# Kernel optimization log

Hardware: AMD Instinct MI355X
Metric: run time of the kernel (lower is better)

## Reference

```python
import jax, jax.numpy as jnp
import numpy as np

B, T, D = 16, 2048, 1024
N_E, D_E = 8, 64


def setup_inputs() -> dict:
    key = jax.random.key(0)
    ks = jax.random.split(key, 8)
    h_seq = jax.random.normal(ks[0], (B, T, D), dtype=jnp.float32)
    entity_keys = jax.random.normal(ks[1], (N_E, D), dtype=jnp.float32) * 0.02
    # input_proj: Linear(D -> D_E)
    Wi = jax.random.normal(ks[2], (D_E, D), dtype=jnp.float32) * (1.0 / np.sqrt(D))
    bi = jnp.zeros((D_E,), dtype=jnp.float32)
    # GRUCell(D_E, D_E): weight_ih (3*D_E, D_E), weight_hh (3*D_E, D_E)
    s = 1.0 / np.sqrt(D_E)
    W_ih = jax.random.uniform(ks[3], (3 * D_E, D_E), minval=-s, maxval=s, dtype=jnp.float32)
    W_hh = jax.random.uniform(ks[4], (3 * D_E, D_E), minval=-s, maxval=s, dtype=jnp.float32)
    b_ih = jax.random.uniform(ks[5], (3 * D_E,), minval=-s, maxval=s, dtype=jnp.float32)
    b_hh = jax.random.uniform(ks[6], (3 * D_E,), minval=-s, maxval=s, dtype=jnp.float32)
    e0 = jnp.zeros((N_E, D_E), dtype=jnp.float32)
    return {"h_seq": h_seq, "entity_keys": entity_keys, "Wi": Wi, "bi": bi,
            "W_ih": W_ih, "W_hh": W_hh, "b_ih": b_ih, "b_hh": b_hh, "e0": e0}


def _entity_scan(h_seq, entity_keys, Wi, bi, W_ih, W_hh, b_ih, b_hh, e0):
    Bq, Tq, Dq = h_seq.shape
    d_e = e0.shape[-1]
    h_proj = jnp.einsum('btd,ed->bte', h_seq, Wi) + bi          # (B,T,D_E)
    logits = jnp.einsum('btd,ed->bte', h_seq, entity_keys) / jnp.sqrt(jnp.float32(Dq))
    route_w = jax.nn.softmax(logits, axis=-1)                    # (B,T,N_E)

    def step(state, xs):
        w_t, hp_t = xs                                           # (B,N_E), (B,D_E)
        inp = w_t[:, :, None] * hp_t[:, None, :]                 # (B,N_E,D_E)
        gx = jnp.einsum('bnd,gd->bng', inp, W_ih) + b_ih         # (B,N_E,3*D_E)
        gh = jnp.einsum('bnd,gd->bng', state, W_hh) + b_hh
        r = jax.nn.sigmoid(gx[..., :d_e] + gh[..., :d_e])
        z = jax.nn.sigmoid(gx[..., d_e:2 * d_e] + gh[..., d_e:2 * d_e])
        n = jnp.tanh(gx[..., 2 * d_e:] + r * gh[..., 2 * d_e:])
        new = (1.0 - z) * n + z * state
        return new, new

    init = jnp.broadcast_to(e0[None], (Bq,) + e0.shape)
    xs = (jnp.swapaxes(route_w, 0, 1), jnp.swapaxes(h_proj, 0, 1))  # time-major
    _, stack = jax.lax.scan(step, init, xs)                      # (T,B,N_E,D_E)
    entity_stack = jnp.swapaxes(stack, 0, 1)                     # (B,T,N_E,D_E)
    entity_seq = entity_stack.reshape(Bq, Tq, -1)                # concat read mode
    return entity_seq, entity_stack


def reference(h_seq, entity_keys, Wi, bi, W_ih, W_hh, b_ih, b_hh, e0):
    return _entity_scan(h_seq, entity_keys, Wi, bi, W_ih, W_hh, b_ih, b_hh, e0)
```

## Files before the change

kernel.cpp:

```cpp
#include <hip/hip_runtime.h>
#include <hip/hip_bf16.h>


constexpr int B_  = 16;
constexpr int T_  = 2048;
constexpr int D_  = 1024;
constexpr int NE  = 8;
constexpr int DE  = 64;
constexpr int G3  = 192;
constexpr int ROWS = B_ * T_;
constexpr int OUT1OFF = ROWS * NE * DE;

typedef __attribute__((ext_vector_type(2))) float f32x2;
typedef __attribute__((ext_vector_type(4))) float f32x4;

__device__ __forceinline__ void pkacc(f32x2& acc, f32x2 w, f32x2 s) {
    asm("v_pk_fma_f32 %0, %1, %2, %0" : "+v"(acc) : "v"(w), "v"(s));
}

__global__ __launch_bounds__(256) void wt_kernel(
    const float* __restrict__ Wi, float* __restrict__ WT4)
{
    const int o  = blockIdx.x;
    const int dq = threadIdx.x;
    const float4 v = *(const float4*)&Wi[o * D_ + dq * 4];
    *(float4*)&WT4[(dq * 64 + o) * 4] = v;
}

constexpr int RPB = 32;
constexpr int CH  = 128;

__global__ __launch_bounds__(256) void proj_kernel(
    const float* __restrict__ h,   const float* __restrict__ ek,
    const float* __restrict__ WT4, const float* __restrict__ bi,
    const float* __restrict__ Wih,
    float* __restrict__ Pout, float* __restrict__ wout)
{
    __shared__ float hch[RPB][CH];
    __shared__ float hp[RPB][DE];
    __shared__ float lg[RPB][NE];

    const int tid = threadIdx.x;
    const int brow = blockIdx.x * RPB;
    const int w = tid >> 6;
    const int o = tid & 63;
    const int n  = o & 7;
    const int sl = o >> 3;

    float acc[8], accl[8];
#pragma unroll
    for (int r = 0; r < 8; ++r) { acc[r] = 0.f; accl[r] = 0.f; }

    for (int kc = 0; kc < D_; kc += CH) {
        __syncthreads();
#pragma unroll
        for (int i = 0; i < 4; ++i) {
            int idx = tid + i * 256;
            int lr = idx >> 5;
            int c4 = (idx & 31) * 4;
            *(float4*)&hch[lr][c4] =
                *(const float4*)&h[(size_t)(brow + lr) * D_ + kc + c4];
        }
        __syncthreads();

        for (int d4 = 0; d4 < CH / 4; ++d4) {
            const float4 wt = *(const float4*)&WT4[((kc >> 2) + d4) * 256 + (o << 2)];
#pragma unroll
            for (int r = 0; r < 8; ++r) {
                const float4 h4 = *(const float4*)&hch[w * 8 + r][d4 * 4];
                acc[r] = fmaf(wt.x, h4.x,
                         fmaf(wt.y, h4.y,
                         fmaf(wt.z, h4.z,
                         fmaf(wt.w, h4.w, acc[r]))));
            }
        }
#pragma unroll
        for (int i4 = 0; i4 < 4; ++i4) {
            const int dl = sl * 16 + i4 * 4;
            const float4 e4 = *(const float4*)&ek[n * D_ + kc + dl];
#pragma unroll
            for (int r = 0; r < 8; ++r) {
                const float4 h4 = *(const float4*)&hch[w * 8 + r][dl];
                accl[r] = fmaf(e4.x, h4.x,
                          fmaf(e4.y, h4.y,
                          fmaf(e4.z, h4.z,
                          fmaf(e4.w, h4.w, accl[r]))));
            }
        }
    }

    const float biv = bi[o];
#pragma unroll
    for (int r = 0; r < 8; ++r) hp[w * 8 + r][o] = acc[r] + biv;

#pragma unroll
    for (int r = 0; r < 8; ++r) {
        accl[r] += __shfl_xor(accl[r], 8);
        accl[r] += __shfl_xor(accl[r], 16);
        accl[r] += __shfl_xor(accl[r], 32);
    }
    if (sl == 0) {
#pragma unroll
        for (int r = 0; r < 8; ++r) lg[w * 8 + r][n] = accl[r] * 0.03125f;
    }
    __syncthreads();

    if (tid < RPB) {
        const int lr = tid;
        float v[NE];
        float m = -1e30f;
#pragma unroll
        for (int e = 0; e < NE; ++e) { v[e] = lg[lr][e]; m = fmaxf(m, v[e]); }
        float s = 0.f;
#pragma unroll
        for (int e = 0; e < NE; ++e) { v[e] = __expf(v[e] - m); s += v[e]; }
        const float inv = 1.f / s;
#pragma unroll
        for (int e = 0; e < NE; ++e)
            wout[(size_t)(brow + lr) * NE + e] = v[e] * inv;
    }

    if (tid < G3) {
        const int k = tid;
        for (int lr0 = 0; lr0 < RPB; lr0 += 8) {
            float pacc[8];
#pragma unroll
            for (int r = 0; r < 8; ++r) pacc[r] = 0.f;
            for (int d4 = 0; d4 < DE / 4; ++d4) {
                const float4 wv = *(const float4*)&Wih[k * DE + d4 * 4];
#pragma unroll
                for (int r = 0; r < 8; ++r) {
                    const float4 h4 = *(const float4*)&hp[lr0 + r][d4 * 4];
                    pacc[r] = fmaf(wv.x, h4.x,
                              fmaf(wv.y, h4.y,
                              fmaf(wv.z, h4.z,
                              fmaf(wv.w, h4.w, pacc[r]))));
                }
            }
#pragma unroll
            for (int r = 0; r < 8; ++r)
                Pout[(size_t)(brow + lr0 + r) * G3 + k] = pacc[r];
        }
    }
}

#define DW(pre, base, q) \
    const f32x4 pre##q = *(const f32x4*)&Whh[(size_t)(base + j) * 64 + 4 * q];
#define DW16(pre, base) \
    DW(pre, base, 0)  DW(pre, base, 1)  DW(pre, base, 2)  DW(pre, base, 3)  \
    DW(pre, base, 4)  DW(pre, base, 5)  DW(pre, base, 6)  DW(pre, base, 7)  \
    DW(pre, base, 8)  DW(pre, base, 9)  DW(pre, base, 10) DW(pre, base, 11) \
    DW(pre, base, 12) DW(pre, base, 13) DW(pre, base, 14) DW(pre, base, 15)

#define MACQ(q) { \
    const f32x4 s4 = *(const f32x4*)&s_l[4 * (q)]; \
    const f32x2 lo = s4.lo, hi = s4.hi; \
    pkacc(aR, wr##q.lo, lo); pkacc(aR, wr##q.hi, hi); \
    pkacc(aZ, wz##q.lo, lo); pkacc(aZ, wz##q.hi, hi); \
    pkacc(aN, wn##q.lo, lo); pkacc(aN, wn##q.hi, hi); }
#define MAC16() \
    MACQ(0)  MACQ(1)  MACQ(2)  MACQ(3)  MACQ(4)  MACQ(5)  MACQ(6)  MACQ(7) \
    MACQ(8)  MACQ(9)  MACQ(10) MACQ(11) MACQ(12) MACQ(13) MACQ(14) MACQ(15)

__global__ __launch_bounds__(64, 1) void scan_kernel(
    const float* __restrict__ P,   const float* __restrict__ route,
    const float* __restrict__ Whh, const float* __restrict__ bih,
    const float* __restrict__ bhh, const float* __restrict__ e0,
    float* __restrict__ out)
{
    __shared__ __align__(16) float s_l[DE];

    const int g   = blockIdx.x;
    const int xcd = g & 7;
    const int ii  = g >> 3;
    const int b   = xcd + 8 * (ii & 1);
    const int n   = ii >> 1;
    const int j   = threadIdx.x;

    DW16(wr, 0)
    DW16(wz, 64)
    DW16(wn, 128)

    const float Br   = bih[j] + bhh[j];
    const float Bz   = bih[64 + j] + bhh[64 + j];
    const float bin_ = bih[128 + j];
    const float bhn_ = bhh[128 + j];

    const size_t row0 = (size_t)b * T_;
    float s_reg = e0[n * DE + j];
    s_l[j] = s_reg;

    const float* Pb = P + row0 * G3;
    const float* wb = route + row0 * NE + n;
    float* op = out + row0 * (size_t)(NE * DE) + n * DE + j;

    float pr0 = Pb[j],            pr1 = Pb[G3 + j];
    float pz0 = Pb[64 + j],       pz1 = Pb[G3 + 64 + j];
    float pn0 = Pb[128 + j],      pn1 = Pb[G3 + 128 + j];
    float wv0 = wb[0],            wv1 = wb[NE];

    for (int t0 = 0; t0 < T_; t0 += 2) {
        const int tb = (t0 + 2 < T_) ? (t0 + 2) : t0;
        const float qr0 = Pb[(size_t)(tb) * G3 + j];
        const float qz0 = Pb[(size_t)(tb) * G3 + 64 + j];
        const float qn0 = Pb[(size_t)(tb) * G3 + 128 + j];
        const float qw0 = wb[tb * NE];
        const float qr1 = Pb[(size_t)(tb + 1) * G3 + j];
        const float qz1 = Pb[(size_t)(tb + 1) * G3 + 64 + j];
        const float qn1 = Pb[(size_t)(tb + 1) * G3 + 128 + j];
        const float qw1 = wb[(tb + 1) * NE];

#pragma unroll
        for (int i = 0; i < 2; ++i) {
            const float pri = i ? pr1 : pr0;
            const float pzi = i ? pz1 : pz0;
            const float pni = i ? pn1 : pn0;
            const float wvi = i ? wv1 : wv0;

            f32x2 aR = {0.f, 0.f}, aZ = {0.f, 0.f}, aN = {0.f, 0.f};
            MAC16()

            const float argR = (aR.x + aR.y) + fmaf(wvi, pri, Br);
            const float argZ = (aZ.x + aZ.y) + fmaf(wvi, pzi, Bz);
            const float rr = __builtin_amdgcn_rcpf(1.f + __expf(-argR));
            const float zz = __builtin_amdgcn_rcpf(1.f + __expf(-argZ));
            const float u  = fmaf(wvi, pni, bin_);
            const float v  = (aN.x + aN.y) + bhn_;
            const float x  = fmaf(rr, v, u);
            const float nn = fmaf(2.f, __builtin_amdgcn_rcpf(1.f + __expf(-2.f * x)), -1.f);
            const float snew = fmaf(zz, s_reg - nn, nn);
            s_reg = snew;
            s_l[j] = snew;
            op[(size_t)(t0 + i) * (NE * DE)] = snew;
        }

        pr0 = qr0; pz0 = qz0; pn0 = qn0; wv0 = qw0;
        pr1 = qr1; pz1 = qz1; pn1 = qn1; wv1 = qw1;
    }
}

__global__ __launch_bounds__(256) void copy_kernel(
    const float4* __restrict__ src, float4* __restrict__ dst, int n4)
{
    int i = blockIdx.x * 256 + threadIdx.x;
    const int stride = gridDim.x * 256;
    for (; i < n4; i += stride) dst[i] = src[i];
}

extern "C" void kernel_launch(void* const* d_in, const int* in_sizes, int n_in,
                              void* d_out, int out_size, void* d_ws, size_t ws_size,
                              hipStream_t stream) {
    const float* h_seq = (const float*)d_in[0];
    const float* ek    = (const float*)d_in[1];
    const float* Wi    = (const float*)d_in[2];
    const float* bi    = (const float*)d_in[3];
    const float* Wih   = (const float*)d_in[4];
    const float* Whh   = (const float*)d_in[5];
    const float* bih   = (const float*)d_in[6];
    const float* bhh   = (const float*)d_in[7];
    const float* e0    = (const float*)d_in[8];
    float* out = (float*)d_out;

    const size_t need = (size_t)ROWS * (G3 + NE) * sizeof(float)
                      + (size_t)DE * D_ * sizeof(float);
    float* wbuf;
    if (ws_size >= need) {
        wbuf = (float*)d_ws;
    } else {
        wbuf = out + OUT1OFF;
    }
    float* Pbuf = wbuf + (size_t)ROWS * NE;
    float* WT4  = Pbuf + (size_t)ROWS * G3;

    wt_kernel<<<DE, 256, 0, stream>>>(Wi, WT4);
    proj_kernel<<<ROWS / RPB, 256, 0, stream>>>(h_seq, ek, WT4, bi, Wih, Pbuf, wbuf);
    scan_kernel<<<B_ * NE, 64, 0, stream>>>(Pbuf, wbuf, Whh, bih, bhh, e0, out);
    copy_kernel<<<2048, 256, 0, stream>>>((const float4*)out, (float4*)(out + OUT1OFF),
                                          OUT1OFF / 4);
}
```

Baseline: 1.121 ms.

## Split GRU gates across three wavefronts and write both outputs directly from scan

The scan kernel now runs 192 threads per block, one wavefront per gate (r, z, n). Each wavefront computes a single 64-wide mat-vec with its gate weights held in registers, and the gates are exchanged through double-buffered shared memory with one barrier per timestep. This cuts the serial per-step work per lane to a third, at the cost of a block-wide barrier on every step. When the workspace is large enough, the second wavefront also writes the duplicate output, so the separate copy kernel is skipped.

```diff
diff --git a/kernel.cpp b/kernel.cpp
--- a/kernel.cpp
+++ b/kernel.cpp
@@ -144,98 +144,92 @@
     }
 }
 
-#define DW(pre, base, q) \
-    const f32x4 pre##q = *(const f32x4*)&Whh[(size_t)(base + j) * 64 + 4 * q];
-#define DW16(pre, base) \
-    DW(pre, base, 0)  DW(pre, base, 1)  DW(pre, base, 2)  DW(pre, base, 3)  \
-    DW(pre, base, 4)  DW(pre, base, 5)  DW(pre, base, 6)  DW(pre, base, 7)  \
-    DW(pre, base, 8)  DW(pre, base, 9)  DW(pre, base, 10) DW(pre, base, 11) \
-    DW(pre, base, 12) DW(pre, base, 13) DW(pre, base, 14) DW(pre, base, 15)
+#define DW(q) const f32x4 w##q = *(const f32x4*)&Whh[(size_t)base * 64 + 4 * (q)];
+#define DW16() \
+    DW(0)  DW(1)  DW(2)  DW(3)  DW(4)  DW(5)  DW(6)  DW(7) \
+    DW(8)  DW(9)  DW(10) DW(11) DW(12) DW(13) DW(14) DW(15)
 
 #define MACQ(q) { \
-    const f32x4 s4 = *(const f32x4*)&s_l[4 * (q)]; \
-    const f32x2 lo = s4.lo, hi = s4.hi; \
-    pkacc(aR, wr##q.lo, lo); pkacc(aR, wr##q.hi, hi); \
-    pkacc(aZ, wz##q.lo, lo); pkacc(aZ, wz##q.hi, hi); \
-    pkacc(aN, wn##q.lo, lo); pkacc(aN, wn##q.hi, hi); }
+    const f32x4 s4 = *(const f32x4*)&s_own[wid][4 * (q)]; \
+    pkacc(acc, w##q.lo, s4.lo); pkacc(acc, w##q.hi, s4.hi); }
 #define MAC16() \
     MACQ(0)  MACQ(1)  MACQ(2)  MACQ(3)  MACQ(4)  MACQ(5)  MACQ(6)  MACQ(7) \
     MACQ(8)  MACQ(9)  MACQ(10) MACQ(11) MACQ(12) MACQ(13) MACQ(14) MACQ(15)
 
-__global__ __launch_bounds__(64, 1) void scan_kernel(
+__global__ __launch_bounds__(192, 1) void scan_kernel(
     const float* __restrict__ P,   const float* __restrict__ route,
     const float* __restrict__ Whh, const float* __restrict__ bih,
     const float* __restrict__ bhh, const float* __restrict__ e0,
-    float* __restrict__ out)
-{
-    __shared__ __align__(16) float s_l[DE];
+    float* __restrict__ out, int write1)
+{
+    __shared__ __align__(16) float s_own[3][DE];
+    __shared__ float ex[2][4][DE];
 
     const int g   = blockIdx.x;
     const int xcd = g & 7;
     const int ii  = g >> 3;
     const int b   = xcd + 8 * (ii & 1);
     const int n   = ii >> 1;
-    const int j   = threadIdx.x;
-
-    DW16(wr, 0)
-    DW16(wz, 64)
-    DW16(wn, 128)
-
-    const float Br   = bih[j] + bhh[j];
-    const float Bz   = bih[64 + j] + bhh[64 + j];
-    const float bin_ = bih[128 + j];
-    const float bhn_ = bhh[128 + j];
+    const int tid = threadIdx.x;
+    const int wid = tid >> 6;
+    const int j   = tid & 63;
+    const int base = wid * DE + j;
+
+    DW16()
+
+    const float Bc   = bih[base] + bhh[base];
+    const float bin_ = bih[base];
+    const float bhn_ = bhh[base];
 
     const size_t row0 = (size_t)b * T_;
     float s_reg = e0[n * DE + j];
-    s_l[j] = s_reg;
-
-    const float* Pb = P + row0 * G3;
-    const float* wb = route + row0 * NE + n;
+    s_own[wid][j] = s_reg;
+
+    const float* Pb = P + row0 * G3 + base;
+    const float* rb = route + row0 * NE + n;
     float* op = out + row0 * (size_t)(NE * DE) + n * DE + j;
 
-    float pr0 = Pb[j],            pr1 = Pb[G3 + j];
-    float pz0 = Pb[64 + j],       pz1 = Pb[G3 + 64 + j];
-    float pn0 = Pb[128 + j],      pn1 = Pb[G3 + 128 + j];
-    float wv0 = wb[0],            wv1 = wb[NE];
-
-    for (int t0 = 0; t0 < T_; t0 += 2) {
-        const int tb = (t0 + 2 < T_) ? (t0 + 2) : t0;
-        const float qr0 = Pb[(size_t)(tb) * G3 + j];
-        const float qz0 = Pb[(size_t)(tb) * G3 + 64 + j];
-        const float qn0 = Pb[(size_t)(tb) * G3 + 128 + j];
-        const float qw0 = wb[tb * NE];
-        const float qr1 = Pb[(size_t)(tb + 1) * G3 + j];
-        const float qz1 = Pb[(size_t)(tb + 1) * G3 + 64 + j];
-        const float qn1 = Pb[(size_t)(tb + 1) * G3 + 128 + j];
-        const float qw1 = wb[(tb + 1) * NE];
-
-#pragma unroll
-        for (int i = 0; i < 2; ++i) {
-            const float pri = i ? pr1 : pr0;
-            const float pzi = i ? pz1 : pz0;
-            const float pni = i ? pn1 : pn0;
-            const float wvi = i ? wv1 : wv0;
-
-            f32x2 aR = {0.f, 0.f}, aZ = {0.f, 0.f}, aN = {0.f, 0.f};
-            MAC16()
-
-            const float argR = (aR.x + aR.y) + fmaf(wvi, pri, Br);
-            const float argZ = (aZ.x + aZ.y) + fmaf(wvi, pzi, Bz);
-            const float rr = __builtin_amdgcn_rcpf(1.f + __expf(-argR));
-            const float zz = __builtin_amdgcn_rcpf(1.f + __expf(-argZ));
-            const float u  = fmaf(wvi, pni, bin_);
-            const float v  = (aN.x + aN.y) + bhn_;
-            const float x  = fmaf(rr, v, u);
-            const float nn = fmaf(2.f, __builtin_amdgcn_rcpf(1.f + __expf(-2.f * x)), -1.f);
-            const float snew = fmaf(zz, s_reg - nn, nn);
-            s_reg = snew;
-            s_l[j] = snew;
-            op[(size_t)(t0 + i) * (NE * DE)] = snew;
-        }
-
-        pr0 = qr0; pz0 = qz0; pn0 = qn0; wv0 = qw0;
-        pr1 = qr1; pz1 = qz1; pn1 = qn1; wv1 = qw1;
+    float p0 = Pb[0], p1 = Pb[G3];
+    float wv0 = rb[0], wv1 = rb[NE];
+
+    int buf = 0;
+
+    for (int t = 0; t < T_; ++t) {
+        const int tn = (t + 2 < T_) ? (t + 2) : t;
+        const float pnx  = Pb[(size_t)tn * G3];
+        const float wnx  = rb[(size_t)tn * NE];
+
+        f32x2 acc = {0.f, 0.f};
+        MAC16()
+        const float gh = acc.x + acc.y;
+        const float gx = fmaf(wv0, p0, (wid == 2) ? bin_ : Bc);
+
+        if (wid == 2) {
+            ex[buf][2][j] = gx;
+            ex[buf][3][j] = gh + bhn_;
+        } else {
+            const float sg = __builtin_amdgcn_rcpf(1.f + __expf(-(gx + gh)));
+            ex[buf][wid][j] = sg;
+        }
+
+        asm volatile("s_waitcnt lgkmcnt(0)" ::: "memory");
+        __builtin_amdgcn_s_barrier();
+
+        const float rr = ex[buf][0][j];
+        const float zz = ex[buf][1][j];
+        const float u  = ex[buf][2][j];
+        const float v  = ex[buf][3][j];
+        const float x  = fmaf(rr, v, u);
+        const float nn = fmaf(2.f, __builtin_amdgcn_rcpf(1.f + __expf(-2.f * x)), -1.f);
+        const float snew = fmaf(zz, s_reg - nn, nn);
+        s_reg = snew;
+        s_own[wid][j] = snew;
+
+        if (wid == 0) op[(size_t)t * (NE * DE)] = snew;
+        else if (write1 && wid == 1) op[OUT1OFF + (size_t)t * (NE * DE)] = snew;
+
+        p0 = p1; p1 = pnx; wv0 = wv1; wv1 = wnx;
+        buf ^= 1;
     }
 }
 
@@ -264,17 +258,23 @@
     const size_t need = (size_t)ROWS * (G3 + NE) * sizeof(float)
                       + (size_t)DE * D_ * sizeof(float);
     float* wbuf;
+    int write1;
     if (ws_size >= need) {
         wbuf = (float*)d_ws;
+        write1 = 1;
     } else {
         wbuf = out + OUT1OFF;
+        write1 = 0;
     }
     float* Pbuf = wbuf + (size_t)ROWS * NE;
     float* WT4  = Pbuf + (size_t)ROWS * G3;
 
     wt_kernel<<<DE, 256, 0, stream>>>(Wi, WT4);
     proj_kernel<<<ROWS / RPB, 256, 0, stream>>>(h_seq, ek, WT4, bi, Wih, Pbuf, wbuf);
-    scan_kernel<<<B_ * NE, 64, 0, stream>>>(Pbuf, wbuf, Whh, bih, bhh, e0, out);
-    copy_kernel<<<2048, 256, 0, stream>>>((const float4*)out, (float4*)(out + OUT1OFF),
-                                          OUT1OFF / 4);
-}
+    scan_kernel<<<B_ * NE, 192, 0, stream>>>(Pbuf, wbuf, Whh, bih, bhh, e0, out, write1);
+
+    if (!write1) {
+        copy_kernel<<<2048, 256, 0, stream>>>((const float4*)out,
+                                              (float4*)(out + OUT1OFF), OUT1OFF / 4);
+    }
+}
```

New measurement: 1.386 ms. 1.24x slower.

## Write both scan outputs directly and split FMA accumulator chains

Applied to the files above, without the earlier changes.

The scan kernel now writes each new state to both output tensors when the workspace is large enough, so the separate copy kernel launch and its full read and write pass over the output are skipped. The packed-FMA accumulators are split into two independent chains per gate to shorten the serial dependency in the recurrent matvec. Empty asm constraints pin the W_hh weights in registers, and launch bounds move to a waves-per-EU attribute. In exchange the serial scan issues twice as many global stores, which may slow its critical path.

```diff
diff --git a/kernel.cpp b/kernel.cpp
--- a/kernel.cpp
+++ b/kernel.cpp
@@ -145,28 +145,36 @@
 }
 
 #define DW(pre, base, q) \
-    const f32x4 pre##q = *(const f32x4*)&Whh[(size_t)(base + j) * 64 + 4 * q];
+    f32x4 pre##q = *(const f32x4*)&Whh[(size_t)(base + j) * 64 + 4 * (q)];
 #define DW16(pre, base) \
     DW(pre, base, 0)  DW(pre, base, 1)  DW(pre, base, 2)  DW(pre, base, 3)  \
     DW(pre, base, 4)  DW(pre, base, 5)  DW(pre, base, 6)  DW(pre, base, 7)  \
     DW(pre, base, 8)  DW(pre, base, 9)  DW(pre, base, 10) DW(pre, base, 11) \
     DW(pre, base, 12) DW(pre, base, 13) DW(pre, base, 14) DW(pre, base, 15)
 
+#define KA(pre, q) asm volatile("" : "+v"(pre##q));
+#define KA16(pre) \
+    KA(pre, 0)  KA(pre, 1)  KA(pre, 2)  KA(pre, 3)  KA(pre, 4)  KA(pre, 5) \
+    KA(pre, 6)  KA(pre, 7)  KA(pre, 8)  KA(pre, 9)  KA(pre, 10) KA(pre, 11) \
+    KA(pre, 12) KA(pre, 13) KA(pre, 14) KA(pre, 15)
+
 #define MACQ(q) { \
     const f32x4 s4 = *(const f32x4*)&s_l[4 * (q)]; \
     const f32x2 lo = s4.lo, hi = s4.hi; \
-    pkacc(aR, wr##q.lo, lo); pkacc(aR, wr##q.hi, hi); \
-    pkacc(aZ, wz##q.lo, lo); pkacc(aZ, wz##q.hi, hi); \
-    pkacc(aN, wn##q.lo, lo); pkacc(aN, wn##q.hi, hi); }
+    pkacc(aRa, wr##q.lo, lo); pkacc(aRb, wr##q.hi, hi); \
+    pkacc(aZa, wz##q.lo, lo); pkacc(aZb, wz##q.hi, hi); \
+    pkacc(aNa, wn##q.lo, lo); pkacc(aNb, wn##q.hi, hi); }
 #define MAC16() \
     MACQ(0)  MACQ(1)  MACQ(2)  MACQ(3)  MACQ(4)  MACQ(5)  MACQ(6)  MACQ(7) \
     MACQ(8)  MACQ(9)  MACQ(10) MACQ(11) MACQ(12) MACQ(13) MACQ(14) MACQ(15)
 
-__global__ __launch_bounds__(64, 1) void scan_kernel(
+__global__ __launch_bounds__(64)
+__attribute__((amdgpu_waves_per_eu(1, 1)))
+void scan_kernel(
     const float* __restrict__ P,   const float* __restrict__ route,
     const float* __restrict__ Whh, const float* __restrict__ bih,
     const float* __restrict__ bhh, const float* __restrict__ e0,
-    float* __restrict__ out)
+    float* __restrict__ out, int write1)
 {
     __shared__ __align__(16) float s_l[DE];
 
@@ -180,6 +188,7 @@
     DW16(wr, 0)
     DW16(wz, 64)
     DW16(wn, 128)
+    KA16(wr) KA16(wz) KA16(wn)
 
     const float Br   = bih[j] + bhh[j];
     const float Bz   = bih[64 + j] + bhh[64 + j];
@@ -194,10 +203,10 @@
     const float* wb = route + row0 * NE + n;
     float* op = out + row0 * (size_t)(NE * DE) + n * DE + j;
 
-    float pr0 = Pb[j],            pr1 = Pb[G3 + j];
-    float pz0 = Pb[64 + j],       pz1 = Pb[G3 + 64 + j];
-    float pn0 = Pb[128 + j],      pn1 = Pb[G3 + 128 + j];
-    float wv0 = wb[0],            wv1 = wb[NE];
+    float pr0 = Pb[j],       pr1 = Pb[G3 + j];
+    float pz0 = Pb[64 + j],  pz1 = Pb[G3 + 64 + j];
+    float pn0 = Pb[128 + j], pn1 = Pb[G3 + 128 + j];
+    float wv0 = wb[0],       wv1 = wb[NE];
 
     for (int t0 = 0; t0 < T_; t0 += 2) {
         const int tb = (t0 + 2 < T_) ? (t0 + 2) : t0;
@@ -217,9 +226,12 @@
             const float pni = i ? pn1 : pn0;
             const float wvi = i ? wv1 : wv0;
 
-            f32x2 aR = {0.f, 0.f}, aZ = {0.f, 0.f}, aN = {0.f, 0.f};
+            f32x2 aRa = {0.f, 0.f}, aRb = {0.f, 0.f};
+            f32x2 aZa = {0.f, 0.f}, aZb = {0.f, 0.f};
+            f32x2 aNa = {0.f, 0.f}, aNb = {0.f, 0.f};
             MAC16()
 
+            const f32x2 aR = aRa + aRb, aZ = aZa + aZb, aN = aNa + aNb;
             const float argR = (aR.x + aR.y) + fmaf(wvi, pri, Br);
             const float argZ = (aZ.x + aZ.y) + fmaf(wvi, pzi, Bz);
             const float rr = __builtin_amdgcn_rcpf(1.f + __expf(-argR));
@@ -232,6 +244,7 @@
             s_reg = snew;
             s_l[j] = snew;
             op[(size_t)(t0 + i) * (NE * DE)] = snew;
+            if (write1) op[OUT1OFF + (size_t)(t0 + i) * (NE * DE)] = snew;
         }
 
         pr0 = qr0; pz0 = qz0; pn0 = qn0; wv0 = qw0;
@@ -264,17 +277,23 @@
     const size_t need = (size_t)ROWS * (G3 + NE) * sizeof(float)
                       + (size_t)DE * D_ * sizeof(float);
     float* wbuf;
+    int write1;
     if (ws_size >= need) {
         wbuf = (float*)d_ws;
+        write1 = 1;
     } else {
         wbuf = out + OUT1OFF;
+        write1 = 0;
     }
     float* Pbuf = wbuf + (size_t)ROWS * NE;
     float* WT4  = Pbuf + (size_t)ROWS * G3;
 
     wt_kernel<<<DE, 256, 0, stream>>>(Wi, WT4);
     proj_kernel<<<ROWS / RPB, 256, 0, stream>>>(h_seq, ek, WT4, bi, Wih, Pbuf, wbuf);
-    scan_kernel<<<B_ * NE, 64, 0, stream>>>(Pbuf, wbuf, Whh, bih, bhh, e0, out);
-    copy_kernel<<<2048, 256, 0, stream>>>((const float4*)out, (float4*)(out + OUT1OFF),
-                                          OUT1OFF / 4);
-}
+    scan_kernel<<<B_ * NE, 64, 0, stream>>>(Pbuf, wbuf, Whh, bih, bhh, e0, out, write1);
+
+    if (!write1) {
+        copy_kernel<<<2048, 256, 0, stream>>>((const float4*)out,
+                                              (float4*)(out + OUT1OFF), OUT1OFF / 4);
+    }
+}
```

After: 1.447 ms. 1.29x slower.

## Restructure projection kernel to hold h rows in registers and drop weight transpose

Applied to the files above, without the earlier changes.

The projection kernel now assigns each thread one row with a quarter of the D dimension, keeping 64 floats of h in registers while looping over the 72 output columns (Wi plus entity keys), which are read as wave-uniform broadcasts. Partial sums across the four waves are combined with shared-memory atomics, and the W_ih projection runs per row from registers. The separate Wi transpose kernel and its workspace are removed. The intent is to drop the LDS staging and one launch, at the cost of high register pressure from the large register arrays and atomic contention in LDS.

```diff
diff --git a/kernel.cpp b/kernel.cpp
--- a/kernel.cpp
+++ b/kernel.cpp
@@ -18,134 +18,104 @@
     asm("v_pk_fma_f32 %0, %1, %2, %0" : "+v"(acc) : "v"(w), "v"(s));
 }
 
-__global__ __launch_bounds__(256) void wt_kernel(
-    const float* __restrict__ Wi, float* __restrict__ WT4)
-{
-    const int o  = blockIdx.x;
-    const int dq = threadIdx.x;
-    const float4 v = *(const float4*)&Wi[o * D_ + dq * 4];
-    *(float4*)&WT4[(dq * 64 + o) * 4] = v;
-}
-
-constexpr int RPB = 32;
-constexpr int CH  = 128;
+constexpr int PRJ_ROWS = 64;
 
 __global__ __launch_bounds__(256) void proj_kernel(
     const float* __restrict__ h,   const float* __restrict__ ek,
-    const float* __restrict__ WT4, const float* __restrict__ bi,
+    const float* __restrict__ Wi,  const float* __restrict__ bi,
     const float* __restrict__ Wih,
     float* __restrict__ Pout, float* __restrict__ wout)
 {
-    __shared__ float hch[RPB][CH];
-    __shared__ float hp[RPB][DE];
-    __shared__ float lg[RPB][NE];
-
-    const int tid = threadIdx.x;
-    const int brow = blockIdx.x * RPB;
-    const int w = tid >> 6;
-    const int o = tid & 63;
-    const int n  = o & 7;
-    const int sl = o >> 3;
-
-    float acc[8], accl[8];
-#pragma unroll
-    for (int r = 0; r < 8; ++r) { acc[r] = 0.f; accl[r] = 0.f; }
-
-    for (int kc = 0; kc < D_; kc += CH) {
-        __syncthreads();
-#pragma unroll
-        for (int i = 0; i < 4; ++i) {
-            int idx = tid + i * 256;
-            int lr = idx >> 5;
-            int c4 = (idx & 31) * 4;
-            *(float4*)&hch[lr][c4] =
-                *(const float4*)&h[(size_t)(brow + lr) * D_ + kc + c4];
-        }
-        __syncthreads();
-
-        for (int d4 = 0; d4 < CH / 4; ++d4) {
-            const float4 wt = *(const float4*)&WT4[((kc >> 2) + d4) * 256 + (o << 2)];
-#pragma unroll
-            for (int r = 0; r < 8; ++r) {
-                const float4 h4 = *(const float4*)&hch[w * 8 + r][d4 * 4];
-                acc[r] = fmaf(wt.x, h4.x,
-                         fmaf(wt.y, h4.y,
-                         fmaf(wt.z, h4.z,
-                         fmaf(wt.w, h4.w, acc[r]))));
+    __shared__ float hp_l[72][PRJ_ROWS];
+
+    const int tid  = threadIdx.x;
+    const int w    = tid >> 6;
+    const int r    = tid & 63;
+    const int brow = blockIdx.x * PRJ_ROWS;
+
+    for (int i = tid; i < 72 * PRJ_ROWS; i += 256) ((float*)hp_l)[i] = 0.f;
+    __syncthreads();
+
+    const float* hrow = h + (size_t)(brow + r) * D_ + w * 256;
+
+    for (int kc = 0; kc < 4; ++kc) {
+        float4 hs[16];
+#pragma unroll
+        for (int i = 0; i < 16; ++i)
+            hs[i] = *(const float4*)&hrow[kc * 64 + i * 4];
+
+        for (int o = 0; o < 72; ++o) {
+            const float* wrow = (o < 64)
+                ? (Wi  + (size_t)o * D_        + w * 256 + kc * 64)
+                : (ek  + (size_t)(o - 64) * D_ + w * 256 + kc * 64);
+            float a0 = 0.f, a1 = 0.f, a2 = 0.f, a3 = 0.f;
+#pragma unroll
+            for (int i = 0; i < 16; i += 4) {
+                const float4 w0 = *(const float4*)&wrow[(i + 0) * 4];
+                const float4 w1 = *(const float4*)&wrow[(i + 1) * 4];
+                const float4 w2 = *(const float4*)&wrow[(i + 2) * 4];
+                const float4 w3 = *(const float4*)&wrow[(i + 3) * 4];
+                a0 = fmaf(w0.x, hs[i+0].x, fmaf(w0.y, hs[i+0].y,
+                     fmaf(w0.z, hs[i+0].z, fmaf(w0.w, hs[i+0].w, a0))));
+                a1 = fmaf(w1.x, hs[i+1].x, fmaf(w1.y, hs[i+1].y,
+                     fmaf(w1.z, hs[i+1].z, fmaf(w1.w, hs[i+1].w, a1))));
+                a2 = fmaf(w2.x, hs[i+2].x, fmaf(w2.y, hs[i+2].y,
+                     fmaf(w2.z, hs[i+2].z, fmaf(w2.w, hs[i+2].w, a2))));
+                a3 = fmaf(w3.x, hs[i+3].x, fmaf(w3.y, hs[i+3].y,
+                     fmaf(w3.z, hs[i+3].z, fmaf(w3.w, hs[i+3].w, a3))));
             }
-        }
-#pragma unroll
-        for (int i4 = 0; i4 < 4; ++i4) {
-            const int dl = sl * 16 + i4 * 4;
-            const float4 e4 = *(const float4*)&ek[n * D_ + kc + dl];
-#pragma unroll
-            for (int r = 0; r < 8; ++r) {
-                const float4 h4 = *(const float4*)&hch[w * 8 + r][dl];
-                accl[r] = fmaf(e4.x, h4.x,
-                          fmaf(e4.y, h4.y,
-                          fmaf(e4.z, h4.z,
-                          fmaf(e4.w, h4.w, accl[r]))));
-            }
-        }
-    }
-
-    const float biv = bi[o];
-#pragma unroll
-    for (int r = 0; r < 8; ++r) hp[w * 8 + r][o] = acc[r] + biv;
-
-#pragma unroll
-    for (int r = 0; r < 8; ++r) {
-        accl[r] += __shfl_xor(accl[r], 8);
-        accl[r] += __shfl_xor(accl[r], 16);
-        accl[r] += __shfl_xor(accl[r], 32);
-    }
-    if (sl == 0) {
-#pragma unroll
-        for (int r = 0; r < 8; ++r) lg[w * 8 + r][n] = accl[r] * 0.03125f;
+            atomicAdd(&hp_l[o][r], (a0 + a1) + (a2 + a3));
+        }
     }
     __syncthreads();
 
-    if (tid < RPB) {
-        const int lr = tid;
+    if (tid < PRJ_ROWS) {
         float v[NE];
         float m = -1e30f;
 #pragma unroll
-        for (int e = 0; e < NE; ++e) { v[e] = lg[lr][e]; m = fmaxf(m, v[e]); }
+        for (int e = 0; e < NE; ++e) {
+            v[e] = hp_l[64 + e][tid] * 0.03125f;
+            m = fmaxf(m, v[e]);
+        }
         float s = 0.f;
 #pragma unroll
         for (int e = 0; e < NE; ++e) { v[e] = __expf(v[e] - m); s += v[e]; }
         const float inv = 1.f / s;
 #pragma unroll
         for (int e = 0; e < NE; ++e)
-            wout[(size_t)(brow + lr) * NE + e] = v[e] * inv;
-    }
-
-    if (tid < G3) {
-        const int k = tid;
-        for (int lr0 = 0; lr0 < RPB; lr0 += 8) {
-            float pacc[8];
-#pragma unroll
-            for (int r = 0; r < 8; ++r) pacc[r] = 0.f;
-            for (int d4 = 0; d4 < DE / 4; ++d4) {
-                const float4 wv = *(const float4*)&Wih[k * DE + d4 * 4];
-#pragma unroll
-                for (int r = 0; r < 8; ++r) {
-                    const float4 h4 = *(const float4*)&hp[lr0 + r][d4 * 4];
-                    pacc[r] = fmaf(wv.x, h4.x,
-                              fmaf(wv.y, h4.y,
-                              fmaf(wv.z, h4.z,
-                              fmaf(wv.w, h4.w, pacc[r]))));
-                }
-            }
-#pragma unroll
-            for (int r = 0; r < 8; ++r)
-                Pout[(size_t)(brow + lr0 + r) * G3 + k] = pacc[r];
-        }
+            wout[(size_t)(brow + tid) * NE + e] = v[e] * inv;
+    }
+
+    float hpr[DE];
+#pragma unroll
+    for (int k = 0; k < DE; ++k)
+        hpr[k] = hp_l[k][r] + bi[k];
+
+    float* prow = Pout + (size_t)(brow + r) * G3;
+    for (int o2 = 48 * w; o2 < 48 * w + 48; ++o2) {
+        const float* wr2 = Wih + (size_t)o2 * DE;
+        float a0 = 0.f, a1 = 0.f, a2 = 0.f, a3 = 0.f;
+#pragma unroll
+        for (int i = 0; i < 16; i += 4) {
+            const float4 w0 = *(const float4*)&wr2[(i + 0) * 4];
+            const float4 w1 = *(const float4*)&wr2[(i + 1) * 4];
+            const float4 w2 = *(const float4*)&wr2[(i + 2) * 4];
+            const float4 w3 = *(const float4*)&wr2[(i + 3) * 4];
+            a0 = fmaf(w0.x, hpr[(i+0)*4+0], fmaf(w0.y, hpr[(i+0)*4+1],
+                 fmaf(w0.z, hpr[(i+0)*4+2], fmaf(w0.w, hpr[(i+0)*4+3], a0))));
+            a1 = fmaf(w1.x, hpr[(i+1)*4+0], fmaf(w1.y, hpr[(i+1)*4+1],
+                 fmaf(w1.z, hpr[(i+1)*4+2], fmaf(w1.w, hpr[(i+1)*4+3], a1))));
+            a2 = fmaf(w2.x, hpr[(i+2)*4+0], fmaf(w2.y, hpr[(i+2)*4+1],
+                 fmaf(w2.z, hpr[(i+2)*4+2], fmaf(w2.w, hpr[(i+2)*4+3], a2))));
+            a3 = fmaf(w3.x, hpr[(i+3)*4+0], fmaf(w3.y, hpr[(i+3)*4+1],
+                 fmaf(w3.z, hpr[(i+3)*4+2], fmaf(w3.w, hpr[(i+3)*4+3], a3))));
+        }
+        prow[o2] = (a0 + a1) + (a2 + a3);
     }
 }
 
 #define DW(pre, base, q) \
-    const f32x4 pre##q = *(const f32x4*)&Whh[(size_t)(base + j) * 64 + 4 * q];
+    const f32x4 pre##q = *(const f32x4*)&Whh[(size_t)(base + j) * 64 + 4 * (q)];
 #define DW16(pre, base) \
     DW(pre, base, 0)  DW(pre, base, 1)  DW(pre, base, 2)  DW(pre, base, 3)  \
     DW(pre, base, 4)  DW(pre, base, 5)  DW(pre, base, 6)  DW(pre, base, 7)  \
@@ -261,8 +231,7 @@
     const float* e0    = (const float*)d_in[8];
     float* out = (float*)d_out;
 
-    const size_t need = (size_t)ROWS * (G3 + NE) * sizeof(float)
-                      + (size_t)DE * D_ * sizeof(float);
+    const size_t need = (size_t)ROWS * (G3 + NE) * sizeof(float);
     float* wbuf;
     if (ws_size >= need) {
         wbuf = (float*)d_ws;
@@ -270,10 +239,8 @@
         wbuf = out + OUT1OFF;
     }
     float* Pbuf = wbuf + (size_t)ROWS * NE;
-    float* WT4  = Pbuf + (size_t)ROWS * G3;
-
-    wt_kernel<<<DE, 256, 0, stream>>>(Wi, WT4);
-    proj_kernel<<<ROWS / RPB, 256, 0, stream>>>(h_seq, ek, WT4, bi, Wih, Pbuf, wbuf);
+
+    proj_kernel<<<ROWS / PRJ_ROWS, 256, 0, stream>>>(h_seq, ek, Wi, bi, Wih, Pbuf, wbuf);
     scan_kernel<<<B_ * NE, 64, 0, stream>>>(Pbuf, wbuf, Whh, bih, bhh, e0, out);
     copy_kernel<<<2048, 256, 0, stream>>>((const float4*)out, (float4*)(out + OUT1OFF),
                                           OUT1OFF / 4);
```

Result: slower. 1.182 ms (+5.4%).
